# Performance work log

Hardware: AMD Instinct MI355X
Metric: run time of the kernel (lower is better)

## Reference

```python
import jax, jax.numpy as jnp
import numpy as np

HIDDEN = 256
ACTIONS = 8
FEAT = 256
N, T = 64, 1024


def _orthogonal(key, shape, scale):
    # hk.initializers.Orthogonal(sqrt(2)) equivalent
    n_rows, n_cols = shape
    big = max(n_rows, n_cols)
    m = jax.random.normal(key, (big, big), dtype=jnp.float32)
    q, r = jnp.linalg.qr(m)
    q = q * jnp.sign(jnp.diag(r))
    return scale * q[:n_rows, :n_cols]


def setup_inputs() -> dict:
    key = jax.random.key(0)
    ks = jax.random.split(key, 8)
    x = jax.random.normal(ks[0], (N, T, FEAT), dtype=jnp.float32)
    a = jax.random.normal(ks[1], (N, T, ACTIONS), dtype=jnp.float32)
    reset = jax.random.randint(ks[2], (N, T), 0, 2).astype(bool)
    s = np.sqrt(2).astype(np.float32)
    w_i = _orthogonal(ks[3], (FEAT, 3 * HIDDEN), s)
    w_h = _orthogonal(ks[4], (HIDDEN, 3 * HIDDEN), s)
    w_a = _orthogonal(ks[5], (ACTIONS, 3 * HIDDEN), s)
    b = jnp.zeros((3 * HIDDEN,), dtype=jnp.float32)
    initial_h = jnp.zeros((HIDDEN,), dtype=jnp.float32)
    return {"x": x, "a": a, "reset": reset, "w_i": w_i, "w_h": w_h,
            "w_a": w_a, "b": b, "initial_h": initial_h}


def reference(x, a, reset, w_i, w_h, w_a, b, initial_h):
    # x: [N,T,F], a: [N,T,A] (one-hot-like), reset: [N,T] bool
    H = initial_h.shape[0]
    w_h_z, w_h_a = w_h[:, :2 * H], w_h[:, 2 * H:]
    b_z, b_a = b[:2 * H], b[2 * H:]
    # Input-side gate projections are time-independent: precompute once.
    gx = jnp.einsum('ntf,fg->ntg', x, w_i)  # [N,T,3H]
    ga = jnp.einsum('nta,ag->ntg', a, w_a)  # [N,T,3H]
    n = x.shape[0]
    h0 = jnp.broadcast_to(initial_h[None, :], (n, H))

    def step(h, inp):
        gx_t, ga_t, r_t = inp  # [N,3H], [N,3H], [N]
        # carry sequence equals learned initial_h (learn_initial_h, is_target=False,
        # carry=None path), so reset restores the learned initial state.
        h = jnp.where(r_t[:, None], initial_h[None, :], h)
        zr = gx_t[:, :2 * H] + ga_t[:, :2 * H] + h @ w_h_z + b_z
        z, r = jnp.split(jax.nn.sigmoid(zr), 2, axis=-1)
        a_t = jnp.tanh(gx_t[:, 2 * H:] + ga_t[:, 2 * H:] + (r * h) @ w_h_a + b_a)
        h_next = (1.0 - z) * h + z * a_t
        return h_next, h_next

    xs = (jnp.swapaxes(gx, 0, 1), jnp.swapaxes(ga, 0, 1), jnp.swapaxes(reset, 0, 1))
    _, hs = jax.lax.scan(step, h0, xs)  # hs: [T,N,H]
    states = jnp.swapaxes(hs, 0, 1)     # [N,T,H]
    outputs = states                    # gru_call returns (next_state, next_state)
    return outputs, states, initial_h[None, :]
```

## Files before the change

kernel.cpp:

```cpp
#include <hip/hip_runtime.h>
#include <hip/hip_fp16.h>

#define NB 64
#define TT 1024
#define FF 256
#define HH 256
#define GG 768
#define AA 8
#define KP 288
#define MM (NB*TT)
#define SGRP 16
#define WCH 16
#define NCH (TT/WCH)
#define LDH 264
#define GSP 776

typedef _Float16 h2v __attribute__((ext_vector_type(2)));
typedef _Float16 v8h __attribute__((ext_vector_type(8)));
typedef float    v4f __attribute__((ext_vector_type(4)));

static __device__ __forceinline__ unsigned pk_rtn(float a, float b) {
    unsigned lo = (unsigned)__half_as_ushort(__float2half(a));
    unsigned hi = (unsigned)__half_as_ushort(__float2half(b));
    return lo | (hi << 16);
}
static __device__ __forceinline__ float h2f(unsigned short u) {
    return (float)__builtin_bit_cast(_Float16, u);
}
static __device__ __forceinline__ unsigned short f2h(float f) {
    return __half_as_ushort(__float2half(f));
}

__global__ __launch_bounds__(1024) void fix_reset(
    const unsigned* __restrict__ src, unsigned char* __restrict__ dst,
    int* __restrict__ Ftab)
{
    __shared__ unsigned red[16];
    const int tid = threadIdx.x;

    unsigned acc = 0;
    #pragma unroll
    for (int i = 0; i < 16; i++)
        acc |= src[tid * 16 + i] & 0xFFFFFF00u;
    #pragma unroll
    for (int off = 32; off >= 1; off >>= 1)
        acc |= __shfl_down(acc, off, 64);
    if ((tid & 63) == 0) red[tid >> 6] = acc;
    __syncthreads();
    unsigned flag = 0;
    #pragma unroll
    for (int i = 0; i < 16; i++) flag |= red[i];
    const bool is_i32 = (flag == 0);

    if (is_i32) {
        const int per = (NB * TT) / 1024;
        #pragma unroll
        for (int i = 0; i < per; i++) {
            int idx = tid * per + i;
            dst[idx] = (unsigned char)(src[idx] != 0 ? 1 : 0);
        }
    } else {
        unsigned* d4 = (unsigned*)dst;
        #pragma unroll
        for (int i = 0; i < 16; i++)
            d4[tid * 16 + i] = src[tid * 16 + i];
    }
    __syncthreads();

    for (int v = tid; v < NB * (NCH + 1); v += 1024) {
        int n = v / (NCH + 1), c = v - n * (NCH + 1);
        int s = TT;
        const unsigned char* r = dst + n * TT;
        for (int t = c * WCH; t < TT; t++)
            if (r[t]) { s = t; break; }
        Ftab[v] = s;
    }
}

__global__ __launch_bounds__(256) void prep_weights(
    const float* __restrict__ w_i, const float* __restrict__ w_a,
    const float* __restrict__ w_h, const float* __restrict__ ihg,
    float* __restrict__ out3,
    unsigned short* __restrict__ wt, unsigned* __restrict__ whb)
{
    const int bid = blockIdx.x;
    if (bid < 865) {
        int idx = bid * 256 + threadIdx.x;
        const int E2 = GG * KP;
        if (idx < E2) {
            int g = idx / KP, k = idx - g * KP;
            float v = 0.f;
            if (k < FF)            v = w_i[k * GG + g];
            else if (k < FF + AA)  v = w_a[(k - FF) * GG + g];
            wt[idx] = f2h(v);
        } else if (idx < E2 + HH) {
            int i = idx - E2;
            out3[i] = ihg[i];
        }
    } else {
        int j = (bid - 865) * 256 + threadIdx.x;
        int w    = j / 12288;
        int r    = j - w * 12288;
        int tile = r >> 8;
        int r2   = r & 255;
        int lane = r2 >> 2, d = r2 & 3;
        int r15 = lane & 15, q = lane >> 4;
        int g, k;
        if (tile < 32) {
            int nt = tile >> 3, kt = tile & 7;
            g = (nt < 2) ? (w * 32 + nt * 16 + r15)
                         : (256 + w * 32 + (nt - 2) * 16 + r15);
            k = kt * 32 + q * 8 + 2 * d;
        } else {
            int t2 = tile - 32;
            int nt2 = t2 >> 3, kt = t2 & 7;
            g = 512 + w * 32 + nt2 * 16 + r15;
            k = kt * 32 + q * 8 + 2 * d;
        }
        whb[j] = pk_rtn(w_h[k * GG + g], w_h[(k + 1) * GG + g]);
    }
}

#define LDK 40

__global__ __launch_bounds__(256, 3) void gemm_fused(
    const float* __restrict__ x, const float* __restrict__ a,
    const unsigned short* __restrict__ wt,
    const float* __restrict__ bias, unsigned short* __restrict__ gxa)
{
    __shared__ __align__(16) unsigned short As[2][128 * LDK];
    __shared__ __align__(16) unsigned short Bs[2][128 * LDK];

    const int bid = blockIdx.x;
    const int wg  = (bid & 7) * 384 + (bid >> 3);
    const int gt = wg % 6, mt = wg / 6;
    const int tid = threadIdx.x;
    const int lane = tid & 63, wv = tid >> 6;
    const int srow = tid & 127, shf = tid >> 7;
    const int r15 = lane & 15, q = lane >> 4;

    v4f acc[2][8];
    #pragma unroll
    for (int i = 0; i < 2; i++)
        #pragma unroll
        for (int j = 0; j < 8; j++) acc[i][j] = (v4f){0.f, 0.f, 0.f, 0.f};

    const int arow = mt * 128 + srow;
    const int brow = gt * 128 + srow;

    float4 f0, f1, f2, f3;
    uint4  pb0, pb1;

    auto issue = [&](int kc) {
        if (kc < 8) {
            const float4* sp = (const float4*)(x + (size_t)arow * FF + kc * 32 + shf * 16);
            f0 = sp[0]; f1 = sp[1]; f2 = sp[2]; f3 = sp[3];
        } else if (shf == 0) {
            const float4* ap = (const float4*)(a + (size_t)arow * AA);
            f0 = ap[0]; f1 = ap[1];
        }
        const uint4* srcB = (const uint4*)(wt + brow * KP + kc * 32 + shf * 16);
        pb0 = srcB[0]; pb1 = srcB[1];
    };
    auto commit = [&](int buf, int kc) {
        uint4 A0, A1;
        if (kc < 8) {
            A0.x = pk_rtn(f0.x, f0.y); A0.y = pk_rtn(f0.z, f0.w);
            A0.z = pk_rtn(f1.x, f1.y); A0.w = pk_rtn(f1.z, f1.w);
            A1.x = pk_rtn(f2.x, f2.y); A1.y = pk_rtn(f2.z, f2.w);
            A1.z = pk_rtn(f3.x, f3.y); A1.w = pk_rtn(f3.z, f3.w);
        } else {
            if (shf == 0) {
                A0.x = pk_rtn(f0.x, f0.y); A0.y = pk_rtn(f0.z, f0.w);
                A0.z = pk_rtn(f1.x, f1.y); A0.w = pk_rtn(f1.z, f1.w);
            } else {
                A0 = (uint4){0, 0, 0, 0};
            }
            A1 = (uint4){0, 0, 0, 0};
        }
        *(uint4*)(As[buf] + srow * LDK + shf * 16)     = A0;
        *(uint4*)(As[buf] + srow * LDK + shf * 16 + 8) = A1;
        *(uint4*)(Bs[buf] + srow * LDK + shf * 16)     = pb0;
        *(uint4*)(Bs[buf] + srow * LDK + shf * 16 + 8) = pb1;
    };

    issue(0);
    commit(0, 0);
    __syncthreads();

    for (int kc = 0; kc < 9; kc++) {
        const int cur = kc & 1;
        if (kc < 8) issue(kc + 1);

        v8h af[2], bf[8];
        #pragma unroll
        for (int mi = 0; mi < 2; mi++)
            af[mi] = *(const v8h*)(As[cur] + (wv * 32 + mi * 16 + r15) * LDK + q * 8);
        #pragma unroll
        for (int nj = 0; nj < 8; nj++)
            bf[nj] = *(const v8h*)(Bs[cur] + (nj * 16 + r15) * LDK + q * 8);
        #pragma unroll
        for (int mi = 0; mi < 2; mi++)
            #pragma unroll
            for (int nj = 0; nj < 8; nj++)
                acc[mi][nj] = __builtin_amdgcn_mfma_f32_16x16x32_f16(
                    af[mi], bf[nj], acc[mi][nj], 0, 0, 0);

        if (kc < 8) {
            commit(cur ^ 1, kc + 1);
            __syncthreads();
        }
    }

    #pragma unroll
    for (int mi = 0; mi < 2; mi++) {
        #pragma unroll
        for (int nj = 0; nj < 8; nj++) {
            int col = gt * 128 + nj * 16 + r15;
            float bv = bias[col];
            #pragma unroll
            for (int v = 0; v < 4; v++) {
                int row = mt * 128 + wv * 32 + mi * 16 + q * 4 + v;
                float val = acc[mi][nj][v] + bv;
                gxa[row * GG + col] = f2h(val);
            }
        }
    }
}

__global__ __launch_bounds__(512, 2) void scan_mfma(
    const unsigned short* __restrict__ gxa, const uint4* __restrict__ whb4,
    const unsigned char* __restrict__ rst, const int* __restrict__ Ftab,
    const float* __restrict__ ihg, float* __restrict__ out)
{
    __shared__ __align__(16) unsigned short h16[SGRP * LDH];
    __shared__ __align__(16) unsigned short rh16[SGRP * LDH];
    __shared__ __align__(16) unsigned short gstage[2][SGRP * GSP];
    __shared__ __align__(16) uint4 waL[8 * 8 * 64];
    __shared__ int s_tb[SGRP], s_te[SGRP], s_emax;

    const int tid = threadIdx.x;
    const int w = tid >> 6, lane = tid & 63;
    const int r15 = lane & 15, q = lane >> 4;
    const int grp = blockIdx.x >> 6;
    const int c   = blockIdx.x & (NCH - 1);
    const int n0  = grp * SGRP;
    const int S   = c * WCH;

    uint4 wb[40];
    #pragma unroll
    for (int i = 0; i < 40; i++) wb[i] = whb4[(w * 48 + i) * 64 + lane];
    #pragma unroll
    for (int rr = 0; rr < 8; rr++) {
        int f = rr * 512 + tid;
        waL[f] = whb4[(rr * 48 + 40 + (tid >> 6)) * 64 + (tid & 63)];
    }

    if (tid < SGRP) {
        s_tb[tid] = (c == 0) ? 0 : Ftab[(n0 + tid) * (NCH + 1) + c];
        s_te[tid] = Ftab[(n0 + tid) * (NCH + 1) + c + 1];
    }
    if (tid == 0) {
        int m = 0;
        for (int i = 0; i < SGRP; i++) m = max(m, s_te[i]);
        s_emax = m;
    }
    for (int idx = tid; idx < SGRP * HH; idx += 512) {
        int sq = idx >> 8, jj = idx & 255;
        bool rb = (c == 0) || (rst[(n0 + sq) * TT + S] != 0);
        float v = rb ? ihg[jj] : 0.f;
        h16[sq * LDH + jj] = f2h(v);
    }
    const int seqS = tid >> 5, jS = tid & 31;
    {
        const uint4* sp = (const uint4*)(gxa + ((size_t)(n0 + seqS) * TT + S) * GG);
        uint4 g0 = sp[jS], g1 = sp[jS + 32], g2 = sp[jS + 64];
        uint4* dp = (uint4*)(gstage[0] + seqS * GSP);
        dp[jS] = g0; dp[jS + 32] = g1; dp[jS + 64] = g2;
    }
    __syncthreads();
    const int Emax = s_emax;

    const int j0 = w * 32 + r15, j1 = j0 + 16;
    const float ih0 = ihg[j0], ih1 = ihg[j1];

    int   seqi[4];
    int   tbte[4];
    float hcr[8];
    #pragma unroll
    for (int v = 0; v < 4; v++) {
        int sq = q * 4 + v;
        seqi[v] = (n0 + sq) * TT;
        tbte[v] = s_tb[sq] | (s_te[sq] << 16);
        bool rb = (c == 0) || (rst[seqi[v] + S] != 0);
        hcr[v]     = rb ? ih0 : 0.f;
        hcr[4 + v] = rb ? ih1 : 0.f;
    }

    const v4f z4 = {0.f, 0.f, 0.f, 0.f};

    for (int t = S; t < Emax; t++) {
        const int cur = (t - S) & 1, nxt = cur ^ 1;
        const int tn = (t + 1 < TT) ? (t + 1) : (TT - 1);

        uint4 g0, g1, g2;
        {
            const uint4* sp = (const uint4*)(gxa + ((size_t)(n0 + seqS) * TT + tn) * GG);
            g0 = sp[jS]; g1 = sp[jS + 32]; g2 = sp[jS + 64];
        }
        unsigned char rn[4];
        #pragma unroll
        for (int v = 0; v < 4; v++) rn[v] = rst[seqi[v] + tn];

        v4f az0 = z4, az1 = z4, ar0 = z4, ar1 = z4;
        #pragma unroll
        for (int kt = 0; kt < 8; kt++) {
            v8h af = *(const v8h*)(h16 + r15 * LDH + kt * 32 + q * 8);
            az0 = __builtin_amdgcn_mfma_f32_16x16x32_f16(af, __builtin_bit_cast(v8h, wb[kt]),      az0, 0, 0, 0);
            az1 = __builtin_amdgcn_mfma_f32_16x16x32_f16(af, __builtin_bit_cast(v8h, wb[8 + kt]),  az1, 0, 0, 0);
            ar0 = __builtin_amdgcn_mfma_f32_16x16x32_f16(af, __builtin_bit_cast(v8h, wb[16 + kt]), ar0, 0, 0, 0);
            ar1 = __builtin_amdgcn_mfma_f32_16x16x32_f16(af, __builtin_bit_cast(v8h, wb[24 + kt]), ar1, 0, 0, 0);
        }

        const unsigned short* gs = gstage[cur];
        float zs[8];
        #pragma unroll
        for (int v = 0; v < 4; v++) {
            int sq = q * 4 + v;
            int gb = sq * GSP;
            float z0 = az0[v] + h2f(gs[gb + j0]);
            float z1 = az1[v] + h2f(gs[gb + j1]);
            zs[v]     = 1.f / (1.f + __expf(-z0));
            zs[4 + v] = 1.f / (1.f + __expf(-z1));
            float r0 = ar0[v] + h2f(gs[gb + 256 + j0]);
            float r1 = ar1[v] + h2f(gs[gb + 256 + j1]);
            float s0 = 1.f / (1.f + __expf(-r0));
            float s1 = 1.f / (1.f + __expf(-r1));
            rh16[sq * LDH + j0] = f2h(s0 * hcr[v]);
            rh16[sq * LDH + j1] = f2h(s1 * hcr[4 + v]);
        }
        __syncthreads();

        v4f aa0 = z4, aa1 = z4;
        #pragma unroll
        for (int kt = 0; kt < 8; kt++) {
            v8h af = *(const v8h*)(rh16 + r15 * LDH + kt * 32 + q * 8);
            uint4 wv4 = waL[(w * 8 + kt) * 64 + lane];
            aa0 = __builtin_amdgcn_mfma_f32_16x16x32_f16(af, __builtin_bit_cast(v8h, wb[32 + kt]), aa0, 0, 0, 0);
            aa1 = __builtin_amdgcn_mfma_f32_16x16x32_f16(af, __builtin_bit_cast(v8h, wv4),         aa1, 0, 0, 0);
        }

        #pragma unroll
        for (int v = 0; v < 4; v++) {
            int sq = q * 4 + v;
            int gb = sq * GSP;
            int tb = tbte[v] & 0xFFFF, te = tbte[v] >> 16;
            bool wr = (t >= tb) && (t < te);
            int mo = (seqi[v] + t) * HH;
            float u0 = aa0[v] + h2f(gs[gb + 512 + j0]);
            float u1 = aa1[v] + h2f(gs[gb + 512 + j1]);
            float e0 = __expf(2.f * u0), e1 = __expf(2.f * u1);
            float t0 = (e0 - 1.f) / (e0 + 1.f);
            float t1 = (e1 - 1.f) / (e1 + 1.f);
            float hn0 = hcr[v]     + zs[v]     * (t0 - hcr[v]);
            float hn1 = hcr[4 + v] + zs[4 + v] * (t1 - hcr[4 + v]);
            if (wr) {
                out[mo + j0] = hn0;
                out[mo + j1] = hn1;
                out[MM * HH + mo + j0] = hn0;
                out[MM * HH + mo + j1] = hn1;
            }
            bool rb = rn[v] != 0;
            float g0f = rb ? ih0 : hn0;
            float g1f = rb ? ih1 : hn1;
            hcr[v] = g0f; hcr[4 + v] = g1f;
            h16[sq * LDH + j0] = f2h(g0f);
            h16[sq * LDH + j1] = f2h(g1f);
        }

        {
            uint4* dp = (uint4*)(gstage[nxt] + seqS * GSP);
            dp[jS] = g0; dp[jS + 32] = g1; dp[jS + 64] = g2;
        }
        __syncthreads();
    }
}

extern "C" void kernel_launch(void* const* d_in, const int* in_sizes, int n_in,
                              void* d_out, int out_size, void* d_ws, size_t ws_size,
                              hipStream_t stream)
{
    const float* x   = (const float*)d_in[0];
    const float* a   = (const float*)d_in[1];
    const void*  rsv = d_in[2];
    const float* w_i = (const float*)d_in[3];
    const float* w_h = (const float*)d_in[4];
    const float* w_a = (const float*)d_in[5];
    const float* b   = (const float*)d_in[6];
    const float* ih  = (const float*)d_in[7];
    float*       out = (float*)d_out;

    char* ws = (char*)d_ws;
    size_t o = 0;
    unsigned short* gxa  = (unsigned short*)(ws + o); o += (size_t)MM * GG * 2;
    unsigned short* wt   = (unsigned short*)(ws + o); o += (size_t)GG * KP * 2;
    unsigned char*  rst8 = (unsigned char*) (ws + o); o += (size_t)NB * TT;
    unsigned*       whb  = (unsigned*)      (ws + o); o += 98304u * 4;
    int*            Ftab = (int*)           (ws + o);

    fix_reset<<<1, 1024, 0, stream>>>((const unsigned*)rsv, rst8, Ftab);

    prep_weights<<<865 + 384, 256, 0, stream>>>(
        w_i, w_a, w_h, ih, out + (size_t)2 * MM * HH, wt, whb);

    gemm_fused<<<512 * 6, 256, 0, stream>>>(x, a, wt, b, gxa);

    scan_mfma<<<(NB / SGRP) * NCH, 512, 0, stream>>>(
        gxa, (const uint4*)whb, rst8, Ftab, ih, out);
}
```

Baseline: 422.2 us.

## Interleave two time chunks per scan block with halved chunk size

The scan kernel now handles two independent time chunks (c0 and c0+64) per block, using the chunk size halved from 16 to 8. The two chunks' MFMA chains are interleaved so their latency overlaps within each step, and the number of blocks stays at 256. The gate staging is restructured: the z/r slices are rewritten after the step and the candidate slice is held in registers, so a single buffer per chunk replaces double buffering. The cost is more registers and LDS, plus redundant warm-up steps from the shorter chunks, which depend on the reset-derived Ftab window lengths.

```diff
diff --git a/kernel.cpp b/kernel.cpp
--- a/kernel.cpp
+++ b/kernel.cpp
@@ -10,7 +10,7 @@
 #define KP 288
 #define MM (NB*TT)
 #define SGRP 16
-#define WCH 16
+#define WCH 8
 #define NCH (TT/WCH)
 #define LDH 264
 #define GSP 776
@@ -233,154 +233,189 @@
     const unsigned char* __restrict__ rst, const int* __restrict__ Ftab,
     const float* __restrict__ ihg, float* __restrict__ out)
 {
-    __shared__ __align__(16) unsigned short h16[SGRP * LDH];
-    __shared__ __align__(16) unsigned short rh16[SGRP * LDH];
-    __shared__ __align__(16) unsigned short gstage[2][SGRP * GSP];
+    __shared__ __align__(16) unsigned short h16[2][SGRP * LDH];
+    __shared__ __align__(16) unsigned short rh16[2][SGRP * LDH];
+    __shared__ __align__(16) unsigned short gs[2][SGRP * GSP];
     __shared__ __align__(16) uint4 waL[8 * 8 * 64];
-    __shared__ int s_tb[SGRP], s_te[SGRP], s_emax;
+    __shared__ int s_len[2];
 
     const int tid = threadIdx.x;
     const int w = tid >> 6, lane = tid & 63;
     const int r15 = lane & 15, q = lane >> 4;
     const int grp = blockIdx.x >> 6;
-    const int c   = blockIdx.x & (NCH - 1);
+    const int c0  = blockIdx.x & 63;
     const int n0  = grp * SGRP;
-    const int S   = c * WCH;
+    const int S0  = c0 * WCH, S1 = (c0 + 64) * WCH;
 
     uint4 wb[40];
     #pragma unroll
     for (int i = 0; i < 40; i++) wb[i] = whb4[(w * 48 + i) * 64 + lane];
     #pragma unroll
-    for (int rr = 0; rr < 8; rr++) {
-        int f = rr * 512 + tid;
-        waL[f] = whb4[(rr * 48 + 40 + (tid >> 6)) * 64 + (tid & 63)];
-    }
-
-    if (tid < SGRP) {
-        s_tb[tid] = (c == 0) ? 0 : Ftab[(n0 + tid) * (NCH + 1) + c];
-        s_te[tid] = Ftab[(n0 + tid) * (NCH + 1) + c + 1];
-    }
-    if (tid == 0) {
-        int m = 0;
-        for (int i = 0; i < SGRP; i++) m = max(m, s_te[i]);
-        s_emax = m;
-    }
-    for (int idx = tid; idx < SGRP * HH; idx += 512) {
-        int sq = idx >> 8, jj = idx & 255;
-        bool rb = (c == 0) || (rst[(n0 + sq) * TT + S] != 0);
-        float v = rb ? ihg[jj] : 0.f;
-        h16[sq * LDH + jj] = f2h(v);
-    }
-    const int seqS = tid >> 5, jS = tid & 31;
-    {
-        const uint4* sp = (const uint4*)(gxa + ((size_t)(n0 + seqS) * TT + S) * GG);
-        uint4 g0 = sp[jS], g1 = sp[jS + 32], g2 = sp[jS + 64];
-        uint4* dp = (uint4*)(gstage[0] + seqS * GSP);
-        dp[jS] = g0; dp[jS + 32] = g1; dp[jS + 64] = g2;
-    }
-    __syncthreads();
-    const int Emax = s_emax;
+    for (int rr = 0; rr < 8; rr++)
+        waL[rr * 512 + tid] = whb4[(rr * 48 + 40 + (tid >> 6)) * 64 + (tid & 63)];
+
+    if (tid < 32) {
+        int uu = tid >> 4, sq = tid & 15;
+        int cc = c0 + (uu ? 64 : 0);
+        int te = Ftab[(n0 + sq) * (NCH + 1) + cc + 1];
+        #pragma unroll
+        for (int off = 8; off >= 1; off >>= 1)
+            te = max(te, __shfl_xor(te, off, 64));
+        if (sq == 0) s_len[uu] = te - (uu ? S1 : S0);
+    }
+
+    for (int idx = tid; idx < 2 * SGRP * HH; idx += 512) {
+        int u = idx >> 12, r = idx & 4095;
+        int sq = r >> 8, jj = r & 255;
+        int Su = u ? S1 : S0;
+        bool rb = (Su == 0) || (rst[(n0 + sq) * TT + Su] != 0);
+        h16[u][sq * LDH + jj] = f2h(rb ? ihg[jj] : 0.f);
+    }
 
     const int j0 = w * 32 + r15, j1 = j0 + 16;
     const float ih0 = ihg[j0], ih1 = ihg[j1];
 
     int   seqi[4];
-    int   tbte[4];
-    float hcr[8];
+    int   tbte[2][4];
+    float hcr[2][8];
     #pragma unroll
     for (int v = 0; v < 4; v++) {
         int sq = q * 4 + v;
         seqi[v] = (n0 + sq) * TT;
-        tbte[v] = s_tb[sq] | (s_te[sq] << 16);
-        bool rb = (c == 0) || (rst[seqi[v] + S] != 0);
-        hcr[v]     = rb ? ih0 : 0.f;
-        hcr[4 + v] = rb ? ih1 : 0.f;
-    }
-
+        #pragma unroll
+        for (int u = 0; u < 2; u++) {
+            int cc = c0 + (u ? 64 : 0);
+            int Su = u ? S1 : S0;
+            int tb = (cc == 0) ? 0 : Ftab[(n0 + sq) * (NCH + 1) + cc];
+            int te = Ftab[(n0 + sq) * (NCH + 1) + cc + 1];
+            tbte[u][v] = tb | (te << 16);
+            bool rb = (Su == 0) || (rst[seqi[v] + Su] != 0);
+            hcr[u][v]     = rb ? ih0 : 0.f;
+            hcr[u][4 + v] = rb ? ih1 : 0.f;
+        }
+    }
+
+    const int seqS = tid >> 5, jS = tid & 31;
+    uint4 aReg[2];
+    #pragma unroll
+    for (int u = 0; u < 2; u++) {
+        int Su = u ? S1 : S0;
+        const uint4* sp = (const uint4*)(gxa + ((size_t)((n0 + seqS) * TT + Su)) * GG);
+        uint4 z0 = sp[jS], z1 = sp[jS + 32];
+        aReg[u] = sp[jS + 64];
+        uint4* dp = (uint4*)(gs[u] + seqS * GSP);
+        dp[jS] = z0; dp[jS + 32] = z1;
+    }
+    __syncthreads();
+
+    const int L = max(s_len[0], s_len[1]);
     const v4f z4 = {0.f, 0.f, 0.f, 0.f};
-
-    for (int t = S; t < Emax; t++) {
-        const int cur = (t - S) & 1, nxt = cur ^ 1;
-        const int tn = (t + 1 < TT) ? (t + 1) : (TT - 1);
-
-        uint4 g0, g1, g2;
-        {
-            const uint4* sp = (const uint4*)(gxa + ((size_t)(n0 + seqS) * TT + tn) * GG);
-            g0 = sp[jS]; g1 = sp[jS + 32]; g2 = sp[jS + 64];
-        }
-        unsigned char rn[4];
-        #pragma unroll
-        for (int v = 0; v < 4; v++) rn[v] = rst[seqi[v] + tn];
-
-        v4f az0 = z4, az1 = z4, ar0 = z4, ar1 = z4;
+    uint4 zrN0[2], zrN1[2];
+
+    for (int s = 0; s < L; s++) {
+        #pragma unroll
+        for (int u = 0; u < 2; u++)
+            ((uint4*)(gs[u] + seqS * GSP))[64 + jS] = aReg[u];
+
+        v4f az0[2], az1[2], ar0[2], ar1[2];
+        #pragma unroll
+        for (int u = 0; u < 2; u++) { az0[u]=z4; az1[u]=z4; ar0[u]=z4; ar1[u]=z4; }
         #pragma unroll
         for (int kt = 0; kt < 8; kt++) {
-            v8h af = *(const v8h*)(h16 + r15 * LDH + kt * 32 + q * 8);
-            az0 = __builtin_amdgcn_mfma_f32_16x16x32_f16(af, __builtin_bit_cast(v8h, wb[kt]),      az0, 0, 0, 0);
-            az1 = __builtin_amdgcn_mfma_f32_16x16x32_f16(af, __builtin_bit_cast(v8h, wb[8 + kt]),  az1, 0, 0, 0);
-            ar0 = __builtin_amdgcn_mfma_f32_16x16x32_f16(af, __builtin_bit_cast(v8h, wb[16 + kt]), ar0, 0, 0, 0);
-            ar1 = __builtin_amdgcn_mfma_f32_16x16x32_f16(af, __builtin_bit_cast(v8h, wb[24 + kt]), ar1, 0, 0, 0);
-        }
-
-        const unsigned short* gs = gstage[cur];
-        float zs[8];
-        #pragma unroll
-        for (int v = 0; v < 4; v++) {
-            int sq = q * 4 + v;
-            int gb = sq * GSP;
-            float z0 = az0[v] + h2f(gs[gb + j0]);
-            float z1 = az1[v] + h2f(gs[gb + j1]);
-            zs[v]     = 1.f / (1.f + __expf(-z0));
-            zs[4 + v] = 1.f / (1.f + __expf(-z1));
-            float r0 = ar0[v] + h2f(gs[gb + 256 + j0]);
-            float r1 = ar1[v] + h2f(gs[gb + 256 + j1]);
-            float s0 = 1.f / (1.f + __expf(-r0));
-            float s1 = 1.f / (1.f + __expf(-r1));
-            rh16[sq * LDH + j0] = f2h(s0 * hcr[v]);
-            rh16[sq * LDH + j1] = f2h(s1 * hcr[4 + v]);
+            v8h afA = *(const v8h*)(h16[0] + r15 * LDH + kt * 32 + q * 8);
+            v8h afB = *(const v8h*)(h16[1] + r15 * LDH + kt * 32 + q * 8);
+            az0[0] = __builtin_amdgcn_mfma_f32_16x16x32_f16(afA, __builtin_bit_cast(v8h, wb[kt]),      az0[0], 0, 0, 0);
+            az0[1] = __builtin_amdgcn_mfma_f32_16x16x32_f16(afB, __builtin_bit_cast(v8h, wb[kt]),      az0[1], 0, 0, 0);
+            az1[0] = __builtin_amdgcn_mfma_f32_16x16x32_f16(afA, __builtin_bit_cast(v8h, wb[8 + kt]),  az1[0], 0, 0, 0);
+            az1[1] = __builtin_amdgcn_mfma_f32_16x16x32_f16(afB, __builtin_bit_cast(v8h, wb[8 + kt]),  az1[1], 0, 0, 0);
+            ar0[0] = __builtin_amdgcn_mfma_f32_16x16x32_f16(afA, __builtin_bit_cast(v8h, wb[16 + kt]), ar0[0], 0, 0, 0);
+            ar0[1] = __builtin_amdgcn_mfma_f32_16x16x32_f16(afB, __builtin_bit_cast(v8h, wb[16 + kt]), ar0[1], 0, 0, 0);
+            ar1[0] = __builtin_amdgcn_mfma_f32_16x16x32_f16(afA, __builtin_bit_cast(v8h, wb[24 + kt]), ar1[0], 0, 0, 0);
+            ar1[1] = __builtin_amdgcn_mfma_f32_16x16x32_f16(afB, __builtin_bit_cast(v8h, wb[24 + kt]), ar1[1], 0, 0, 0);
+        }
+
+        float zs[2][8];
+        #pragma unroll
+        for (int u = 0; u < 2; u++) {
+            const unsigned short* g = gs[u];
+            #pragma unroll
+            for (int v = 0; v < 4; v++) {
+                int sq = q * 4 + v, gb = sq * GSP;
+                float z0 = az0[u][v] + h2f(g[gb + j0]);
+                float z1 = az1[u][v] + h2f(g[gb + j1]);
+                zs[u][v]     = 1.f / (1.f + __expf(-z0));
+                zs[u][4 + v] = 1.f / (1.f + __expf(-z1));
+                float r0 = ar0[u][v] + h2f(g[gb + 256 + j0]);
+                float r1 = ar1[u][v] + h2f(g[gb + 256 + j1]);
+                float sg0 = 1.f / (1.f + __expf(-r0));
+                float sg1 = 1.f / (1.f + __expf(-r1));
+                rh16[u][sq * LDH + j0] = f2h(sg0 * hcr[u][v]);
+                rh16[u][sq * LDH + j1] = f2h(sg1 * hcr[u][4 + v]);
+            }
         }
         __syncthreads();
 
-        v4f aa0 = z4, aa1 = z4;
+        unsigned char rn[2][4];
+        #pragma unroll
+        for (int u = 0; u < 2; u++) {
+            int trd = min((u ? S1 : S0) + s + 1, TT - 1);
+            const uint4* sp = (const uint4*)(gxa + ((size_t)((n0 + seqS) * TT + trd)) * GG);
+            zrN0[u] = sp[jS]; zrN1[u] = sp[jS + 32]; aReg[u] = sp[jS + 64];
+            #pragma unroll
+            for (int v = 0; v < 4; v++)
+                rn[u][v] = rst[seqi[v] + trd];
+        }
+
+        v4f aa0[2], aa1[2];
+        #pragma unroll
+        for (int u = 0; u < 2; u++) { aa0[u]=z4; aa1[u]=z4; }
         #pragma unroll
         for (int kt = 0; kt < 8; kt++) {
-            v8h af = *(const v8h*)(rh16 + r15 * LDH + kt * 32 + q * 8);
             uint4 wv4 = waL[(w * 8 + kt) * 64 + lane];
-            aa0 = __builtin_amdgcn_mfma_f32_16x16x32_f16(af, __builtin_bit_cast(v8h, wb[32 + kt]), aa0, 0, 0, 0);
-            aa1 = __builtin_amdgcn_mfma_f32_16x16x32_f16(af, __builtin_bit_cast(v8h, wv4),         aa1, 0, 0, 0);
-        }
-
-        #pragma unroll
-        for (int v = 0; v < 4; v++) {
-            int sq = q * 4 + v;
-            int gb = sq * GSP;
-            int tb = tbte[v] & 0xFFFF, te = tbte[v] >> 16;
-            bool wr = (t >= tb) && (t < te);
-            int mo = (seqi[v] + t) * HH;
-            float u0 = aa0[v] + h2f(gs[gb + 512 + j0]);
-            float u1 = aa1[v] + h2f(gs[gb + 512 + j1]);
-            float e0 = __expf(2.f * u0), e1 = __expf(2.f * u1);
-            float t0 = (e0 - 1.f) / (e0 + 1.f);
-            float t1 = (e1 - 1.f) / (e1 + 1.f);
-            float hn0 = hcr[v]     + zs[v]     * (t0 - hcr[v]);
-            float hn1 = hcr[4 + v] + zs[4 + v] * (t1 - hcr[4 + v]);
-            if (wr) {
-                out[mo + j0] = hn0;
-                out[mo + j1] = hn1;
-                out[MM * HH + mo + j0] = hn0;
-                out[MM * HH + mo + j1] = hn1;
+            v8h pfA = *(const v8h*)(rh16[0] + r15 * LDH + kt * 32 + q * 8);
+            v8h pfB = *(const v8h*)(rh16[1] + r15 * LDH + kt * 32 + q * 8);
+            aa0[0] = __builtin_amdgcn_mfma_f32_16x16x32_f16(pfA, __builtin_bit_cast(v8h, wb[32 + kt]), aa0[0], 0, 0, 0);
+            aa0[1] = __builtin_amdgcn_mfma_f32_16x16x32_f16(pfB, __builtin_bit_cast(v8h, wb[32 + kt]), aa0[1], 0, 0, 0);
+            aa1[0] = __builtin_amdgcn_mfma_f32_16x16x32_f16(pfA, __builtin_bit_cast(v8h, wv4),         aa1[0], 0, 0, 0);
+            aa1[1] = __builtin_amdgcn_mfma_f32_16x16x32_f16(pfB, __builtin_bit_cast(v8h, wv4),         aa1[1], 0, 0, 0);
+        }
+
+        #pragma unroll
+        for (int u = 0; u < 2; u++) {
+            const unsigned short* g = gs[u];
+            const int t = (u ? S1 : S0) + s;
+            #pragma unroll
+            for (int v = 0; v < 4; v++) {
+                int sq = q * 4 + v, gb = sq * GSP;
+                int tb = tbte[u][v] & 0xFFFF, te = tbte[u][v] >> 16;
+                bool wr = (t >= tb) && (t < te);
+                int mo = (seqi[v] + t) * HH;
+                float u0 = aa0[u][v] + h2f(g[gb + 512 + j0]);
+                float u1 = aa1[u][v] + h2f(g[gb + 512 + j1]);
+                float e0 = __expf(2.f * u0), e1 = __expf(2.f * u1);
+                float t0 = (e0 - 1.f) / (e0 + 1.f);
+                float t1 = (e1 - 1.f) / (e1 + 1.f);
+                float hn0 = hcr[u][v]     + zs[u][v]     * (t0 - hcr[u][v]);
+                float hn1 = hcr[u][4 + v] + zs[u][4 + v] * (t1 - hcr[u][4 + v]);
+                if (wr) {
+                    out[mo + j0] = hn0;
+                    out[mo + j1] = hn1;
+                    out[MM * HH + mo + j0] = hn0;
+                    out[MM * HH + mo + j1] = hn1;
+                }
+                bool rb = rn[u][v] != 0;
+                float g0f = rb ? ih0 : hn0;
+                float g1f = rb ? ih1 : hn1;
+                hcr[u][v] = g0f; hcr[u][4 + v] = g1f;
+                h16[u][sq * LDH + j0] = f2h(g0f);
+                h16[u][sq * LDH + j1] = f2h(g1f);
             }
-            bool rb = rn[v] != 0;
-            float g0f = rb ? ih0 : hn0;
-            float g1f = rb ? ih1 : hn1;
-            hcr[v] = g0f; hcr[4 + v] = g1f;
-            h16[sq * LDH + j0] = f2h(g0f);
-            h16[sq * LDH + j1] = f2h(g1f);
-        }
-
-        {
-            uint4* dp = (uint4*)(gstage[nxt] + seqS * GSP);
-            dp[jS] = g0; dp[jS + 32] = g1; dp[jS + 64] = g2;
+        }
+
+        #pragma unroll
+        for (int u = 0; u < 2; u++) {
+            uint4* dp = (uint4*)(gs[u] + seqS * GSP);
+            dp[jS] = zrN0[u]; dp[jS + 32] = zrN1[u];
         }
         __syncthreads();
     }
@@ -415,6 +450,6 @@
 
     gemm_fused<<<512 * 6, 256, 0, stream>>>(x, a, wt, b, gxa);
 
-    scan_mfma<<<(NB / SGRP) * NCH, 512, 0, stream>>>(
+    scan_mfma<<<(NB / SGRP) * 64, 512, 0, stream>>>(
         gxa, (const uint4*)whb, rst8, Ftab, ih, out);
 }
```

Result: slower. 573.2 us (+35.8%).
